# Kernel optimization log

Hardware: AMD Instinct MI355X
Metric: run time of the kernel (lower is better)

Reference implementation:

```python
import jax, jax.numpy as jnp
import numpy as np

B, S, DM, L = 128, 168, 128, 2
I, N, R, K, P = 256, 16, 8, 4, 24


def setup_inputs() -> dict:
    key = jax.random.key(0)
    ks = iter(jax.random.split(key, 32))
    rn = lambda shape, s=0.02: jax.random.normal(next(ks), shape, jnp.float32) * s
    return {
        'x_load': jax.random.normal(next(ks), (B, S, 1), jnp.float32),
        'x_img': jax.random.normal(next(ks), (B, S, 64), jnp.float32),
        'x_text': jax.random.normal(next(ks), (B, S, 768), jnp.float32),
        'Wl': rn((DM, 1)), 'Wi': rn((DM, 64)), 'Wt': rn((DM, 768)),
        'b_fuse': jnp.zeros((DM,), jnp.float32),
        'mnorm_w': jnp.ones((L, DM), jnp.float32),
        'in_w': rn((L, 2 * I, DM)), 'in_b': jnp.zeros((L, 2 * I), jnp.float32),
        'conv_w': rn((L, I, K), 0.3), 'conv_b': jnp.zeros((L, I), jnp.float32),
        'xp_w': rn((L, R + 2 * N, I)),
        'dt_w': rn((L, I, R), 0.1), 'dt_b': rn((L, I), 0.1),
        'A_log': rn((L, I, N), 1.0),
        'Dp': jnp.ones((L, I), jnp.float32),
        'out_w': rn((L, DM, I)), 'out_b': jnp.zeros((L, DM), jnp.float32),
        'fnorm_w': jnp.ones((DM,), jnp.float32),
        'ln_w': jnp.ones((DM,), jnp.float32), 'ln_b': jnp.zeros((DM,), jnp.float32),
        'fc_w': rn((P, DM)), 'fc_b': jnp.zeros((P,), jnp.float32),
    }


def rmsnorm(x, w, eps=1e-5):
    return x * jax.lax.rsqrt(jnp.mean(x * x, -1, keepdims=True) + eps) * w


def layernorm(x, w, b, eps=1e-5):
    m = jnp.mean(x, -1, keepdims=True)
    v = jnp.mean((x - m) ** 2, -1, keepdims=True)
    return (x - m) * jax.lax.rsqrt(v + eps) * w + b


def ssm_scan(dA, dBu, C):
    # dA, dBu: [B,S,I,N]; C: [B,S,N] -> y: [B,S,I]
    def step(state, inp):
        dA_s, dBu_s, C_s = inp
        state = dA_s * state + dBu_s                      # [B,I,N]
        y = jnp.einsum('bin,bn->bi', state, C_s)
        return state, y
    init = jnp.zeros_like(dA[:, 0])
    xs = (dA.transpose(1, 0, 2, 3), dBu.transpose(1, 0, 2, 3), C.transpose(1, 0, 2))
    _, ys = jax.lax.scan(step, init, xs)
    return ys.transpose(1, 0, 2)


def mamba_mixer(h, in_w, in_b, conv_w, conv_b, xp_w, dt_w, dt_b, A_log, Dp, out_w, out_b):
    hs_gate = h @ in_w.T + in_b                           # [B,S,2I]
    hs, gate = jnp.split(hs_gate, 2, axis=-1)
    u = hs.transpose(0, 2, 1)                             # [B,I,S]
    pad = jnp.pad(u, ((0, 0), (0, 0), (K - 1, 0)))        # causal depthwise conv
    u = sum(conv_w[None, :, k, None] * pad[:, :, k:k + S] for k in range(K))
    u = jax.nn.silu(u + conv_b[None, :, None])
    ut = u.transpose(0, 2, 1)                             # [B,S,I]
    sp = ut @ xp_w.T                                      # [B,S,R+2N]
    dt_in, Bm, Cm = jnp.split(sp, [R, R + N], axis=-1)
    dt = jax.nn.softplus(dt_in @ dt_w.T + dt_b)           # [B,S,I]
    A = -jnp.exp(A_log)                                   # [I,N]
    dA = jnp.exp(dt[..., None] * A[None, None])           # [B,S,I,N]
    dBu = dt[..., None] * Bm[:, :, None, :] * ut[..., None]
    y = ssm_scan(dA, dBu, Cm)                             # [B,S,I]
    y = y + ut * Dp[None, None, :]
    y = y * jax.nn.silu(gate)
    return y @ out_w.T + out_b


def reference(x_load, x_img, x_text, Wl, Wi, Wt, b_fuse, mnorm_w, in_w, in_b,
              conv_w, conv_b, xp_w, dt_w, dt_b, A_log, Dp, out_w, out_b,
              fnorm_w, ln_w, ln_b, fc_w, fc_b):
    # shared feature fusion -> [B,S,DM]
    h = x_load @ Wl.T + x_img @ Wi.T + x_text @ Wt.T + b_fuse
    for l in range(L):
        h = h + mamba_mixer(rmsnorm(h, mnorm_w[l]), in_w[l], in_b[l], conv_w[l],
                            conv_b[l], xp_w[l], dt_w[l], dt_b[l], A_log[l],
                            Dp[l], out_w[l], out_b[l])
    h = rmsnorm(h, fnorm_w)
    last = layernorm(h[:, -1, :], ln_w, ln_b)
    out = last @ fc_w.T + fc_b                            # [B,P]
    return out[..., None]
```

## Files before the change

kernel.cpp:

```cpp
#include <hip/hip_runtime.h>
#include <hip/hip_bf16.h>

#define BB   128
#define SS   168
#define DM   128
#define LL   2
#define II   256
#define NN   16
#define RR   8
#define KK   4
#define PP   24
#define MROWS (BB*SS)
#define NCH  12
#define TCH  14

#define XPF  24
#define INF  128
#define FR_TOT (LL*(XPF+INF))

typedef __attribute__((ext_vector_type(8))) short bf16x8;
typedef __attribute__((ext_vector_type(4))) short bf16x4;
typedef __attribute__((ext_vector_type(4))) float f32x4;

__device__ __forceinline__ float wave_sum(float x) {
#pragma unroll
    for (int off = 32; off > 0; off >>= 1) x += __shfl_xor(x, off);
    return x;
}
__device__ __forceinline__ float siluf(float x) {
    return x / (1.f + __expf(-x));
}
__device__ __forceinline__ float softplusf(float x) {
    return (x > 20.f) ? x : __logf(1.f + __expf(x));
}
__device__ __forceinline__ short f2bf(float x) {
    unsigned u = __builtin_bit_cast(unsigned, x);
    u = (u + 0x7FFFu + ((u >> 16) & 1u)) >> 16;
    return (short)u;
}
__device__ __forceinline__ bf16x4 pack4(const float* f) {
    bf16x4 r;
#pragma unroll
    for (int j = 0; j < 4; ++j) r[j] = f2bf(f[j]);
    return r;
}
__device__ __forceinline__ bf16x8 pack8(const float* f) {
    bf16x8 r;
#pragma unroll
    for (int j = 0; j < 8; ++j) r[j] = f2bf(f[j]);
    return r;
}
__device__ __forceinline__ bf16x8 cvt8v(float4 a, float4 b) {
    unsigned u0, u1, u2, u3;
    asm("v_cvt_pk_bf16_f32 %0, %1, %2" : "=v"(u0) : "v"(a.x), "v"(a.y));
    asm("v_cvt_pk_bf16_f32 %0, %1, %2" : "=v"(u1) : "v"(a.z), "v"(a.w));
    asm("v_cvt_pk_bf16_f32 %0, %1, %2" : "=v"(u2) : "v"(b.x), "v"(b.y));
    asm("v_cvt_pk_bf16_f32 %0, %1, %2" : "=v"(u3) : "v"(b.z), "v"(b.w));
    union { unsigned u[4]; bf16x8 v; } r;
    r.u[0] = u0; r.u[1] = u1; r.u[2] = u2; r.u[3] = u3;
    return r.v;
}

__global__ __launch_bounds__(256)
void hn_kernel(const float* __restrict__ h, const float* __restrict__ mnw,
               short* __restrict__ hn)
{
    const int row  = blockIdx.x * 4 + (threadIdx.x >> 6);
    const int lane = threadIdx.x & 63;
    const float2 v = *(const float2*)&h[(size_t)row * DM + lane * 2];
    const float ss = wave_sum(v.x * v.x + v.y * v.y);
    const float rsv = rsqrtf(ss * (1.f / DM) + 1e-5f);
    const float2 w = *(const float2*)&mnw[lane * 2];
    short2 o;
    o.x = f2bf(v.x * rsv * w.x);
    o.y = f2bf(v.y * rsv * w.y);
    *(short2*)&hn[(size_t)row * DM + lane * 2] = o;
}

__global__ __launch_bounds__(256)
void cvtw_kernel(const float* __restrict__ xw, const float* __restrict__ inw,
                 short* __restrict__ dst)
{
    const int tid = blockIdx.x * 256 + threadIdx.x;
    if (tid >= FR_TOT * 64) return;
    const int lane = tid & 63;
    const int fg = tid >> 6;
    float4 v0 = {0.f, 0.f, 0.f, 0.f}, v1 = {0.f, 0.f, 0.f, 0.f};
    if (fg < LL * XPF) {
        const int l = fg / XPF, f = fg % XPF;
        const int nt = f >> 3, kt = f & 7;
        const int row = nt * 16 + (lane & 15);
        const int kc = kt * 32 + (lane >> 4) * 8;
        if (row < 40) {
            const float* s = xw + ((size_t)l * 40 + row) * II + kc;
            v0 = *(const float4*)s;
            v1 = *(const float4*)(s + 4);
        }
    } else {
        const int g = fg - LL * XPF;
        const int l = g / INF, fi = g % INF;
        const int nt = fi >> 2, kt = fi & 3;
        const int row = nt * 16 + (lane & 15);
        const int kc = kt * 32 + (lane >> 4) * 8;
        const float* s = inw + ((size_t)l * 2 * II + row) * DM + kc;
        v0 = *(const float4*)s;
        v1 = *(const float4*)(s + 4);
    }
    *(bf16x8*)(dst + ((size_t)tid) * 8) = cvt8v(v0, v1);
}

#define LDT 40
template<bool ACCUM>
__global__ __launch_bounds__(256)
void gemm_mfma(const float* __restrict__ A, const short* __restrict__ Abf,
               const float* __restrict__ W, int K,
               const float* __restrict__ A2, const float* __restrict__ W2, int K2,
               const float* __restrict__ bias,
               const float* __restrict__ r1x, const float* __restrict__ r1w,
               float* __restrict__ C, int ldc)
{
    __shared__ __align__(16) short Asl[32 * LDT];
    __shared__ __align__(16) short Bsl[64 * LDT];
    const int bm = blockIdx.x * 32;
    const int bn = blockIdx.y * 64;
    const int t  = threadIdx.x;
    const int lane = t & 63;
    const int wave = t >> 6;
    const int wr = wave >> 1, wc = wave & 1;
    const int lrow = lane & 15;
    const int lk   = (lane >> 4) * 8;

    f32x4 acc[2];
    acc[0] = (f32x4){0.f, 0.f, 0.f, 0.f};
    acc[1] = (f32x4){0.f, 0.f, 0.f, 0.f};

    const int arow = t >> 3, ak = (t & 7) * 4;
    const int brow = t >> 2, bk = (t & 3) * 8;

    float av[4], bv[8];
    bf16x4 avb;

#pragma unroll 1
    for (int pass = 0; pass < 2; ++pass) {
        const bool useBf = (pass == 0) && (Abf != nullptr);
        const float* Ap = pass ? A2 : A;
        if (!Ap && !useBf) continue;
        const float* Wp = pass ? W2 : W;
        const int    Kp = pass ? K2 : K;
        const short* abptr = useBf ? Abf + (size_t)(bm + arow) * Kp + ak : nullptr;
        const float* aptr  = useBf ? nullptr : Ap + (size_t)(bm + arow) * Kp + ak;
        const float* bptr = Wp + (size_t)(bn + brow) * Kp + bk;

        if (useBf) avb = *(const bf16x4*)(abptr);
        else       *(float4*)&av[0] = *(const float4*)(aptr);
        *(float4*)&bv[0] = *(const float4*)(bptr);
        *(float4*)&bv[4] = *(const float4*)(bptr + 4);

#pragma unroll 1
        for (int k0 = 0; k0 < Kp; k0 += 32) {
            __syncthreads();
            if (useBf) *(bf16x4*)&Asl[arow * LDT + ak] = avb;
            else       *(bf16x4*)&Asl[arow * LDT + ak] = pack4(av);
            *(bf16x8*)&Bsl[brow * LDT + bk] = pack8(bv);
            __syncthreads();
            const int kn = k0 + 32;
            if (kn < Kp) {
                if (useBf) avb = *(const bf16x4*)(abptr + kn);
                else       *(float4*)&av[0] = *(const float4*)(aptr + kn);
                *(float4*)&bv[0] = *(const float4*)(bptr + kn);
                *(float4*)&bv[4] = *(const float4*)(bptr + kn + 4);
            }
            const bf16x8 af = *(const bf16x8*)&Asl[(wr * 16 + lrow) * LDT + lk];
            bf16x8 bfr[2];
#pragma unroll
            for (int ni = 0; ni < 2; ++ni)
                bfr[ni] = *(const bf16x8*)&Bsl[(wc * 32 + ni * 16 + lrow) * LDT + lk];
#pragma unroll
            for (int ni = 0; ni < 2; ++ni)
                acc[ni] = __builtin_amdgcn_mfma_f32_16x16x32_bf16(af, bfr[ni], acc[ni], 0, 0, 0);
        }
    }

#pragma unroll
    for (int r = 0; r < 4; ++r) {
        const int row = bm + wr * 16 + (lane >> 4) * 4 + r;
        const float xl = r1x ? r1x[row] : 0.f;
#pragma unroll
        for (int ni = 0; ni < 2; ++ni) {
            const int col = bn + wc * 32 + ni * 16 + lrow;
            float v = acc[ni][r];
            if (bias) v += bias[col];
            if (r1x)  v += xl * r1w[col];
            float* cp = &C[(size_t)row * ldc + col];
            if (ACCUM) v += *cp;
            *cp = v;
        }
    }
}

__global__ __launch_bounds__(256)
void fusedA_kernel(const short* __restrict__ hn, const float* __restrict__ cw,
                   const float* __restrict__ cb, const short* __restrict__ inws,
                   const short* __restrict__ xws, const float* __restrict__ inb,
                   const float* __restrict__ dtw, const float* __restrict__ dtb,
                   const float* __restrict__ A_log,
                   float* __restrict__ ut, float* __restrict__ sp,
                   float* __restrict__ dtsum_g, float* __restrict__ q)
{
    __shared__ float hsl[17][II + 4];
    __shared__ float uts[TCH][II + 4];
    __shared__ float lsp[TCH * 40];
    const int b = blockIdx.x;
    const int ch = blockIdx.y;
    const int i = threadIdx.x;
    const int s0 = ch * TCH;
    const int lane = i & 63;
    const int wv = i >> 6;
    const int lrow = lane & 15;
    const int lkg = (lane >> 4) * 8;
    const int r0 = (lane >> 4) * 4;

    {
        const short* hnb = hn + (size_t)b * SS * DM;
#pragma unroll
        for (int mt = 0; mt < 2; ++mt) {
            const int ma = mt * 16 + lrow;
            const int rga = s0 - 3 + ma;
            const bool va = (ma < 17) && (rga >= 0);
            bf16x8 af[4];
#pragma unroll
            for (int kt = 0; kt < 4; ++kt) {
                if (va) af[kt] = *(const bf16x8*)(hnb + (size_t)rga * DM + kt * 32 + lkg);
                else { bf16x8 z = {0,0,0,0,0,0,0,0}; af[kt] = z; }
            }
#pragma unroll
            for (int j = 0; j < 4; ++j) {
                const int nt = wv * 4 + j;
                f32x4 acc = (f32x4){0.f, 0.f, 0.f, 0.f};
#pragma unroll
                for (int kt = 0; kt < 4; ++kt) {
                    const bf16x8 bf = *(const bf16x8*)(inws + ((size_t)(nt * 4 + kt) * 64 + lane) * 8);
                    acc = __builtin_amdgcn_mfma_f32_16x16x32_bf16(af[kt], bf, acc, 0, 0, 0);
                }
                const int n = nt * 16 + lrow;
                const float bn_ = inb[n];
#pragma unroll
                for (int r = 0; r < 4; ++r) {
                    const int mrow = mt * 16 + r0 + r;
                    if (mrow < 17) {
                        const int rg = s0 - 3 + mrow;
                        hsl[mrow][n] = (rg < 0) ? 0.f : acc[r] + bn_;
                    }
                }
            }
        }
    }
    __syncthreads();

    {
        const float4 w = *(const float4*)&cw[i * 4];
        const float bi = cb[i];
        float* up = ut + (size_t)b * SS * II + i;
        float wm3 = hsl[0][i], wm2 = hsl[1][i], wm1 = hsl[2][i];
        for (int s = 0; s < TCH; ++s) {
            const float cur = hsl[s + 3][i];
            float a = fmaf(w.x, wm3, fmaf(w.y, wm2, fmaf(w.z, wm1, fmaf(w.w, cur, bi))));
            const float uv = siluf(a);
            up[(s0 + s) * II] = uv;
            uts[s][i] = uv;
            wm3 = wm2; wm2 = wm1; wm1 = cur;
        }
    }
    __syncthreads();

    {
        if (wv < 3) {
            const int srow = lrow;
            const short* wp = xws + ((size_t)(wv * 8) * 64 + lane) * 8;
            f32x4 acc = (f32x4){0.f, 0.f, 0.f, 0.f};
#pragma unroll
            for (int kt = 0; kt < 8; ++kt) {
                const float* up = &uts[0][0] + srow * (II + 4) + kt * 32 + lkg;
                const float4 a0 = *(const float4*)(up);
                const float4 a1 = *(const float4*)(up + 4);
                const bf16x8 af = cvt8v(a0, a1);
                const bf16x8 bf = *(const bf16x8*)(wp + (size_t)kt * 512);
                acc = __builtin_amdgcn_mfma_f32_16x16x32_bf16(af, bf, acc, 0, 0, 0);
            }
            const int col = wv * 16 + lrow;
            if (col < 40) {
#pragma unroll
                for (int r = 0; r < 4; ++r)
                    if (r0 + r < TCH) lsp[(r0 + r) * 40 + col] = acc[r];
            }
        }
    }
    __syncthreads();

    {
        float* spp = sp + ((size_t)b * SS + s0) * 40;
        for (int idx = i; idx < TCH * 40; idx += 256) spp[idx] = lsp[idx];
    }

    float dw[8];
    {
        const float4 w0 = *(const float4*)&dtw[i * 8];
        const float4 w1 = *(const float4*)&dtw[i * 8 + 4];
        dw[0]=w0.x; dw[1]=w0.y; dw[2]=w0.z; dw[3]=w0.w;
        dw[4]=w1.x; dw[5]=w1.y; dw[6]=w1.z; dw[7]=w1.w;
    }
    const float bdt = dtb[i];
    float Ar[NN];
#pragma unroll
    for (int n = 0; n < NN; ++n) Ar[n] = -__expf(A_log[i * NN + n]);

    float st[NN];
#pragma unroll
    for (int n = 0; n < NN; ++n) st[n] = 0.f;
    float dtsum = 0.f;

    for (int s = 0; s < TCH; ++s) {
        const float uv = uts[s][i];
        const float* r = &lsp[s * 40];
        const float p0 = fmaf(r[1], dw[1], r[0] * dw[0]);
        const float p1 = fmaf(r[3], dw[3], r[2] * dw[2]);
        const float p2 = fmaf(r[5], dw[5], r[4] * dw[4]);
        const float p3 = fmaf(r[7], dw[7], r[6] * dw[6]);
        const float dtv = softplusf(bdt + (p0 + p1) + (p2 + p3));
        const float du = dtv * uv;
        dtsum += dtv;
#pragma unroll
        for (int n = 0; n < NN; ++n) {
            const float a = __expf(dtv * Ar[n]);
            st[n] = fmaf(a, st[n], du * r[8 + n]);
        }
    }
    dtsum_g[((size_t)b * NCH + ch) * II + i] = dtsum;
    float* qp = q + (((size_t)b * NCH + ch) * NN) * II + i;
#pragma unroll
    for (int n = 0; n < NN; ++n) qp[n * II] = st[n];
}

__global__ __launch_bounds__(256)
void combine_kernel(const float* __restrict__ dtsum_g,
                    const float* __restrict__ A_log, float* __restrict__ q)
{
    const int b = blockIdx.x;
    const int i = threadIdx.x;
    float Ar[NN];
#pragma unroll
    for (int n = 0; n < NN; ++n) Ar[n] = -__expf(A_log[i * NN + n]);
    float ds[NCH];
#pragma unroll
    for (int ch = 0; ch < NCH; ++ch)
        ds[ch] = dtsum_g[((size_t)b * NCH + ch) * II + i];
#pragma unroll
    for (int n = 0; n < NN; ++n) {
        float cur = 0.f;
#pragma unroll
        for (int ch = 0; ch < NCH; ++ch) {
            const size_t idx = (((size_t)b * NCH + ch) * NN + n) * II + i;
            const float Pv = __expf(Ar[n] * ds[ch]);
            const float qv = q[idx];
            q[idx] = cur;
            cur = fmaf(Pv, cur, qv);
        }
    }
}

__global__ __launch_bounds__(256)
void scanB_kernel(const float* __restrict__ ut, const float* __restrict__ sp,
                  const float* __restrict__ qinit, const short* __restrict__ inws,
                  const short* __restrict__ hn, const float* __restrict__ inb,
                  const float* __restrict__ dtw, const float* __restrict__ dtb,
                  const float* __restrict__ A_log, const float* __restrict__ Dp,
                  short* __restrict__ ygb)
{
    __shared__ float gsl[TCH][II + 4];
    __shared__ float lsp[TCH * 40];
    const int b = blockIdx.x;
    const int ch = blockIdx.y;
    const int i = threadIdx.x;
    const int s0 = ch * TCH;
    const int lane = i & 63;
    const int wv = i >> 6;
    const int lrow = lane & 15;
    const int lkg = (lane >> 4) * 8;
    const int r0 = (lane >> 4) * 4;

    {
        const short* hnb = hn + (size_t)b * SS * DM;
        const bool va = (lrow < TCH);
        const int rga = s0 + lrow;
        bf16x8 af[4];
#pragma unroll
        for (int kt = 0; kt < 4; ++kt) {
            if (va) af[kt] = *(const bf16x8*)(hnb + (size_t)rga * DM + kt * 32 + lkg);
            else { bf16x8 z = {0,0,0,0,0,0,0,0}; af[kt] = z; }
        }
#pragma unroll
        for (int j = 0; j < 4; ++j) {
            const int nt = 16 + wv * 4 + j;
            f32x4 acc = (f32x4){0.f, 0.f, 0.f, 0.f};
#pragma unroll
            for (int kt = 0; kt < 4; ++kt) {
                const bf16x8 bf = *(const bf16x8*)(inws + ((size_t)(nt * 4 + kt) * 64 + lane) * 8);
                acc = __builtin_amdgcn_mfma_f32_16x16x32_bf16(af[kt], bf, acc, 0, 0, 0);
            }
            const int n = (nt - 16) * 16 + lrow;
            const float bn_ = inb[256 + n];
#pragma unroll
            for (int r = 0; r < 4; ++r)
                if (r0 + r < TCH) gsl[r0 + r][n] = acc[r] + bn_;
        }
    }

    {
        const float* spp = sp + ((size_t)b * SS + s0) * 40;
        for (int idx = i; idx < TCH * 40; idx += 256) lsp[idx] = spp[idx];
    }
    float dw[8];
    {
        const float4 w0 = *(const float4*)&dtw[i * 8];
        const float4 w1 = *(const float4*)&dtw[i * 8 + 4];
        dw[0]=w0.x; dw[1]=w0.y; dw[2]=w0.z; dw[3]=w0.w;
        dw[4]=w1.x; dw[5]=w1.y; dw[6]=w1.z; dw[7]=w1.w;
    }
    const float bdt = dtb[i];
    const float Dv = Dp[i];
    float Ar[NN];
#pragma unroll
    for (int n = 0; n < NN; ++n) Ar[n] = -__expf(A_log[i * NN + n]);

    float st[NN];
    {
        const float* qp = qinit + (((size_t)b * NCH + ch) * NN) * II + i;
#pragma unroll
        for (int n = 0; n < NN; ++n) st[n] = qp[n * II];
    }

    const float* utp = ut + ((size_t)b * SS + s0) * II + i;
    short* yp = ygb + ((size_t)b * SS + s0) * II + i;
    __syncthreads();

    float uv = utp[0];
    for (int s = 0; s < TCH; ++s) {
        const int sn = (s + 1 < TCH) ? s + 1 : s;
        const float uv_n = utp[sn * II];
        const float* r = &lsp[s * 40];
        const float p0 = fmaf(r[1], dw[1], r[0] * dw[0]);
        const float p1 = fmaf(r[3], dw[3], r[2] * dw[2]);
        const float p2 = fmaf(r[5], dw[5], r[4] * dw[4]);
        const float p3 = fmaf(r[7], dw[7], r[6] * dw[6]);
        const float dtv = softplusf(bdt + (p0 + p1) + (p2 + p3));
        const float du = dtv * uv;
        float y0 = 0.f, y1 = 0.f, y2 = 0.f, y3 = 0.f;
#pragma unroll
        for (int n = 0; n < NN; n += 4) {
            const float a0 = __expf(dtv * Ar[n + 0]);
            const float a1 = __expf(dtv * Ar[n + 1]);
            const float a2 = __expf(dtv * Ar[n + 2]);
            const float a3 = __expf(dtv * Ar[n + 3]);
            st[n + 0] = fmaf(a0, st[n + 0], du * r[8 + n + 0]);
            st[n + 1] = fmaf(a1, st[n + 1], du * r[8 + n + 1]);
            st[n + 2] = fmaf(a2, st[n + 2], du * r[8 + n + 2]);
            st[n + 3] = fmaf(a3, st[n + 3], du * r[8 + n + 3]);
            y0 = fmaf(st[n + 0], r[24 + n + 0], y0);
            y1 = fmaf(st[n + 1], r[24 + n + 1], y1);
            y2 = fmaf(st[n + 2], r[24 + n + 2], y2);
            y3 = fmaf(st[n + 3], r[24 + n + 3], y3);
        }
        const float yv = (y0 + y1) + (y2 + y3) + uv * Dv;
        yp[s * II] = f2bf(yv * siluf(gsl[s][i]));
        uv = uv_n;
    }
}

__global__ __launch_bounds__(64)
void final_kernel(const float* __restrict__ h, const float* __restrict__ fnw,
                  const float* __restrict__ lnw, const float* __restrict__ lnb,
                  const float* __restrict__ fcw, const float* __restrict__ fcb,
                  float* __restrict__ out)
{
    __shared__ float last[DM];
    const int b = blockIdx.x;
    const int lane = threadIdx.x;
    const float* hp = &h[((size_t)b * SS + (SS - 1)) * DM];
    const float2 v = *(const float2*)&hp[lane * 2];
    const float ss = wave_sum(v.x * v.x + v.y * v.y);
    const float sc = rsqrtf(ss * (1.f / DM) + 1e-5f);
    const float2 fw = *(const float2*)&fnw[lane * 2];
    const float t0 = v.x * sc * fw.x, t1 = v.y * sc * fw.y;
    const float m = wave_sum(t0 + t1) * (1.f / DM);
    const float d0 = t0 - m, d1 = t1 - m;
    const float var = wave_sum(d0 * d0 + d1 * d1) * (1.f / DM);
    const float iv = rsqrtf(var + 1e-5f);
    const float2 lw = *(const float2*)&lnw[lane * 2];
    const float2 lb = *(const float2*)&lnb[lane * 2];
    last[lane * 2]     = d0 * iv * lw.x + lb.x;
    last[lane * 2 + 1] = d1 * iv * lw.y + lb.y;
    __syncthreads();
    if (lane < PP) {
        float a = fcb[lane];
#pragma unroll 8
        for (int d = 0; d < DM; ++d) a = fmaf(last[d], fcw[lane * DM + d], a);
        out[b * PP + lane] = a;
    }
}

extern "C" void kernel_launch(void* const* d_in, const int* in_sizes, int n_in,
                              void* d_out, int out_size, void* d_ws, size_t ws_size,
                              hipStream_t stream)
{
    (void)in_sizes; (void)n_in; (void)out_size; (void)ws_size;
    const float* x_load = (const float*)d_in[0];
    const float* x_img  = (const float*)d_in[1];
    const float* x_text = (const float*)d_in[2];
    const float* Wl     = (const float*)d_in[3];
    const float* Wi     = (const float*)d_in[4];
    const float* Wt     = (const float*)d_in[5];
    const float* b_fuse = (const float*)d_in[6];
    const float* mnorm_w= (const float*)d_in[7];
    const float* in_w   = (const float*)d_in[8];
    const float* in_b   = (const float*)d_in[9];
    const float* conv_w = (const float*)d_in[10];
    const float* conv_b = (const float*)d_in[11];
    const float* xp_w   = (const float*)d_in[12];
    const float* dt_w   = (const float*)d_in[13];
    const float* dt_b   = (const float*)d_in[14];
    const float* A_log  = (const float*)d_in[15];
    const float* Dp     = (const float*)d_in[16];
    const float* out_w  = (const float*)d_in[17];
    const float* out_b  = (const float*)d_in[18];
    const float* fnorm_w= (const float*)d_in[19];
    const float* ln_w   = (const float*)d_in[20];
    const float* ln_b   = (const float*)d_in[21];
    const float* fc_w   = (const float*)d_in[22];
    const float* fc_b   = (const float*)d_in[23];

    float* ws  = (float*)d_ws;
    float* h     = ws;
    float* ut    = h  + (size_t)MROWS * DM;
    float* sp    = ut + (size_t)MROWS * II;
    float* q     = sp + (size_t)MROWS * 40;
    float* dtsum = q  + (size_t)BB * NCH * NN * II;
    short* pool  = (short*)(dtsum + (size_t)BB * NCH * II);
    short* hn    = pool + (size_t)FR_TOT * 512;
    short* ygb   = hn + (size_t)MROWS * DM;

    cvtw_kernel<<<(FR_TOT * 64 + 255) / 256, 256, 0, stream>>>(xp_w, in_w, pool);

    gemm_mfma<false><<<dim3(MROWS / 32, 2), 256, 0, stream>>>(
        x_text, nullptr, Wt, 768, x_img, Wi, 64, b_fuse, x_load, Wl,
        h, DM);

    for (int l = 0; l < LL; ++l) {
        const short* xws  = pool + (size_t)l * XPF * 512;
        const short* inws = pool + (size_t)(LL * XPF + l * INF) * 512;
        hn_kernel<<<MROWS / 4, 256, 0, stream>>>(h, mnorm_w + l * DM, hn);
        fusedA_kernel<<<dim3(BB, NCH), 256, 0, stream>>>(
            hn, conv_w + l * II * KK, conv_b + l * II, inws, xws,
            in_b + (size_t)l * 2 * II,
            dt_w + l * II * RR, dt_b + l * II, A_log + l * II * NN,
            ut, sp, dtsum, q);
        combine_kernel<<<BB, 256, 0, stream>>>(dtsum, A_log + l * II * NN, q);
        scanB_kernel<<<dim3(BB, NCH), 256, 0, stream>>>(
            ut, sp, q, inws, hn, in_b + (size_t)l * 2 * II,
            dt_w + l * II * RR, dt_b + l * II,
            A_log + l * II * NN, Dp + l * II, ygb);
        gemm_mfma<true><<<dim3(MROWS / 32, 2), 256, 0, stream>>>(
            nullptr, ygb, out_w + (size_t)l * DM * II, II,
            nullptr, nullptr, 0,
            out_b + l * DM, nullptr, nullptr,
            h, DM);
    }

    final_kernel<<<BB, 64, 0, stream>>>(h, fnorm_w, ln_w, ln_b, fc_w, fc_b,
                                        (float*)d_out);
}
```

Before: 224.1 us.

## Fuse output projection GEMM into scan kernel epilogue with residual add

The gated scan output is kept in shared memory as bf16, and each scan block multiplies its 14-row tile by pre-converted bf16 out_w fragments using MFMA. It then adds the result plus bias directly into the residual h. This removes the separate out-projection GEMM launch and the global round trip of the bf16 y buffer. In exchange, scanB uses more shared memory and does extra MFMA work per block, and the residual is updated with scattered per-element read-modify-write stores.

```diff
diff --git a/kernel.cpp b/kernel.cpp
--- a/kernel.cpp
+++ b/kernel.cpp
@@ -16,7 +16,8 @@
 
 #define XPF  24
 #define INF  128
-#define FR_TOT (LL*(XPF+INF))
+#define OUTF 64
+#define FR_TOT (LL*(XPF+INF+OUTF))
 
 typedef __attribute__((ext_vector_type(8))) short bf16x8;
 typedef __attribute__((ext_vector_type(4))) short bf16x4;
@@ -79,7 +80,7 @@
 
 __global__ __launch_bounds__(256)
 void cvtw_kernel(const float* __restrict__ xw, const float* __restrict__ inw,
-                 short* __restrict__ dst)
+                 const float* __restrict__ outw, short* __restrict__ dst)
 {
     const int tid = blockIdx.x * 256 + threadIdx.x;
     if (tid >= FR_TOT * 64) return;
@@ -96,13 +97,22 @@
             v0 = *(const float4*)s;
             v1 = *(const float4*)(s + 4);
         }
-    } else {
+    } else if (fg < LL * (XPF + INF)) {
         const int g = fg - LL * XPF;
         const int l = g / INF, fi = g % INF;
         const int nt = fi >> 2, kt = fi & 3;
         const int row = nt * 16 + (lane & 15);
         const int kc = kt * 32 + (lane >> 4) * 8;
         const float* s = inw + ((size_t)l * 2 * II + row) * DM + kc;
+        v0 = *(const float4*)s;
+        v1 = *(const float4*)(s + 4);
+    } else {
+        const int g = fg - LL * (XPF + INF);
+        const int l = g / OUTF, fo = g % OUTF;
+        const int nt = fo >> 3, kt = fo & 7;
+        const int row = nt * 16 + (lane & 15);
+        const int kc = kt * 32 + (lane >> 4) * 8;
+        const float* s = outw + ((size_t)l * DM + row) * II + kc;
         v0 = *(const float4*)s;
         v1 = *(const float4*)(s + 4);
     }
@@ -368,16 +378,19 @@
     }
 }
 
+#define YLD 296
 __global__ __launch_bounds__(256)
 void scanB_kernel(const float* __restrict__ ut, const float* __restrict__ sp,
                   const float* __restrict__ qinit, const short* __restrict__ inws,
-                  const short* __restrict__ hn, const float* __restrict__ inb,
+                  const short* __restrict__ outws, const short* __restrict__ hn,
+                  const float* __restrict__ inb, const float* __restrict__ outb,
                   const float* __restrict__ dtw, const float* __restrict__ dtb,
                   const float* __restrict__ A_log, const float* __restrict__ Dp,
-                  short* __restrict__ ygb)
+                  float* __restrict__ h)
 {
     __shared__ float gsl[TCH][II + 4];
     __shared__ float lsp[TCH * 40];
+    __shared__ __align__(16) short ygl[16 * YLD];
     const int b = blockIdx.x;
     const int ch = blockIdx.y;
     const int i = threadIdx.x;
@@ -388,6 +401,8 @@
     const int lkg = (lane >> 4) * 8;
     const int r0 = (lane >> 4) * 4;
 
+    ygl[14 * YLD + i] = 0; ygl[15 * YLD + i] = 0;
+
     {
         const short* hnb = hn + (size_t)b * SS * DM;
         const bool va = (lrow < TCH);
@@ -440,7 +455,6 @@
     }
 
     const float* utp = ut + ((size_t)b * SS + s0) * II + i;
-    short* yp = ygb + ((size_t)b * SS + s0) * II + i;
     __syncthreads();
 
     float uv = utp[0];
@@ -471,8 +485,36 @@
             y3 = fmaf(st[n + 3], r[24 + n + 3], y3);
         }
         const float yv = (y0 + y1) + (y2 + y3) + uv * Dv;
-        yp[s * II] = f2bf(yv * siluf(gsl[s][i]));
+        ygl[s * YLD + i] = f2bf(yv * siluf(gsl[s][i]));
         uv = uv_n;
+    }
+    __syncthreads();
+
+    {
+        bf16x8 af[8];
+#pragma unroll
+        for (int kt = 0; kt < 8; ++kt)
+            af[kt] = *(const bf16x8*)&ygl[lrow * YLD + kt * 32 + lkg];
+#pragma unroll
+        for (int j = 0; j < 2; ++j) {
+            const int nt = wv * 2 + j;
+            f32x4 acc = (f32x4){0.f, 0.f, 0.f, 0.f};
+#pragma unroll
+            for (int kt = 0; kt < 8; ++kt) {
+                const bf16x8 bf = *(const bf16x8*)(outws + ((size_t)(nt * 8 + kt) * 64 + lane) * 8);
+                acc = __builtin_amdgcn_mfma_f32_16x16x32_bf16(af[kt], bf, acc, 0, 0, 0);
+            }
+            const int col = nt * 16 + lrow;
+            const float bo = outb[col];
+#pragma unroll
+            for (int r = 0; r < 4; ++r) {
+                const int srow = r0 + r;
+                if (srow < TCH) {
+                    float* hp = &h[((size_t)b * SS + s0 + srow) * DM + col];
+                    *hp += acc[r] + bo;
+                }
+            }
+        }
     }
 }
 
@@ -546,17 +588,18 @@
     float* dtsum = q  + (size_t)BB * NCH * NN * II;
     short* pool  = (short*)(dtsum + (size_t)BB * NCH * II);
     short* hn    = pool + (size_t)FR_TOT * 512;
-    short* ygb   = hn + (size_t)MROWS * DM;
-
-    cvtw_kernel<<<(FR_TOT * 64 + 255) / 256, 256, 0, stream>>>(xp_w, in_w, pool);
+
+    cvtw_kernel<<<(FR_TOT * 64 + 255) / 256, 256, 0, stream>>>(
+        xp_w, in_w, out_w, pool);
 
     gemm_mfma<false><<<dim3(MROWS / 32, 2), 256, 0, stream>>>(
         x_text, nullptr, Wt, 768, x_img, Wi, 64, b_fuse, x_load, Wl,
         h, DM);
 
     for (int l = 0; l < LL; ++l) {
-        const short* xws  = pool + (size_t)l * XPF * 512;
-        const short* inws = pool + (size_t)(LL * XPF + l * INF) * 512;
+        const short* xws   = pool + (size_t)l * XPF * 512;
+        const short* inws  = pool + (size_t)(LL * XPF + l * INF) * 512;
+        const short* outws = pool + (size_t)(LL * (XPF + INF) + l * OUTF) * 512;
         hn_kernel<<<MROWS / 4, 256, 0, stream>>>(h, mnorm_w + l * DM, hn);
         fusedA_kernel<<<dim3(BB, NCH), 256, 0, stream>>>(
             hn, conv_w + l * II * KK, conv_b + l * II, inws, xws,
@@ -565,14 +608,10 @@
             ut, sp, dtsum, q);
         combine_kernel<<<BB, 256, 0, stream>>>(dtsum, A_log + l * II * NN, q);
         scanB_kernel<<<dim3(BB, NCH), 256, 0, stream>>>(
-            ut, sp, q, inws, hn, in_b + (size_t)l * 2 * II,
+            ut, sp, q, inws, outws, hn,
+            in_b + (size_t)l * 2 * II, out_b + l * DM,
             dt_w + l * II * RR, dt_b + l * II,
-            A_log + l * II * NN, Dp + l * II, ygb);
-        gemm_mfma<true><<<dim3(MROWS / 32, 2), 256, 0, stream>>>(
-            nullptr, ygb, out_w + (size_t)l * DM * II, II,
-            nullptr, nullptr, 0,
-            out_b + l * DM, nullptr, nullptr,
-            h, DM);
+            A_log + l * II * NN, Dp + l * II, h);
     }
 
     final_kernel<<<BB, 64, 0, stream>>>(h, fnorm_w, ln_w, ln_b, fc_w, fc_b,
```

New measurement: 201.8 us. 1.11x faster.
